# Kernel tuning notes

Measured on AMD Instinct MI355X. Metric: run time of the kernel, lower is better.

The kernel has to match this reference:

```python
import jax, jax.numpy as jnp
import numpy as np

H = 128
S = 65  # 64 board cells + 1 appended bias token


def _attn(y, wk, wq, wv):
    # y: [B, H, S]
    k = jnp.einsum('ij,bjs->bis', wk, y)
    q = jnp.einsum('ij,bjs->bis', wq, y)
    v = jnp.einsum('ij,bjs->bis', wv, y)
    kq = jnp.einsum('bis,bit->bst', k, q)          # k.T @ q -> [B, S, S]
    sm = jax.nn.softmax(kq, axis=-1)               # softmax over dim=1 of [S,S]
    return jnp.einsum('bst,bit->bsi', sm, v)       # sm @ v.T -> [B, S, H]


def setup_inputs() -> dict:
    key = jax.random.key(0)
    ks = jax.random.split(key, 17)
    B = 8192
    d = dict(
        inputs=jax.random.normal(ks[0], (1, B, 64), jnp.float32),
        embeding=jax.random.normal(ks[1], (H, S), jnp.float32),
        w_k11=jax.random.normal(ks[2], (H, H), jnp.float32),
        w_q11=jax.random.normal(ks[3], (H, H), jnp.float32),
        w_v11=jax.random.normal(ks[4], (H, H), jnp.float32),
        w_k12=jax.random.normal(ks[5], (H, H), jnp.float32),
        w_q12=jax.random.normal(ks[6], (H, H), jnp.float32),
        w_v12=jax.random.normal(ks[7], (H, H), jnp.float32),
        linear1=jax.random.normal(ks[8], (2 * H, H), jnp.float32),
        w_k21=jax.random.normal(ks[9], (H, H), jnp.float32),
        w_q21=jax.random.normal(ks[10], (H, H), jnp.float32),
        w_v21=jax.random.normal(ks[11], (H, H), jnp.float32),
        w_k22=jax.random.normal(ks[12], (H, H), jnp.float32),
        w_q22=jax.random.normal(ks[13], (H, H), jnp.float32),
        w_v22=jax.random.normal(ks[14], (H, H), jnp.float32),
        linear2=jax.random.normal(ks[15], (2 * H, H), jnp.float32),
        linear3=jax.random.normal(ks[16], (H, H // 2), jnp.float32),
        linear4=jax.random.normal(jax.random.fold_in(key, 99), (H // 2, 1), jnp.float32),
    )
    return d


def reference(inputs, embeding, w_k11, w_q11, w_v11, w_k12, w_q12, w_v12, linear1,
              w_k21, w_q21, w_v21, w_k22, w_q22, w_v22, linear2, linear3, linear4):
    xb = inputs[0]                                   # [B, 64]
    B = xb.shape[0]
    x = jnp.concatenate([xb, jnp.ones((B, 1), xb.dtype)], axis=1)  # [B, 65]
    y = embeding[None, :, :] * x[:, None, :]         # [B, H, S]

    att11 = _attn(y, w_k11, w_q11, w_v11)            # [B, S, H]
    att12 = _attn(y, w_k12, w_q12, w_v12)
    y = jnp.tanh(jnp.concatenate([att11, att12], axis=-1) @ linear1)  # [B, S, H]
    y = jnp.swapaxes(y, 1, 2)                        # [B, H, S]

    att21 = _attn(y, w_k21, w_q21, w_v21)
    att22 = _attn(y, w_k22, w_q22, w_v22)
    y = jnp.tanh(jnp.concatenate([att21, att22], axis=-1) @ linear2)  # [B, S, H]
    y = y[:, 64, :]                                  # take bias token -> [B, H]
    y = jnp.tanh(y @ linear3)                        # [B, H//2]
    score = y @ linear4                              # [B, 1]
    return score[:, 0][None, :]                      # [1, B]
```

## Files before the change

### kernel.cpp

```cpp
#include <hip/hip_runtime.h>
#include <math.h>


#define YQ(s, q) ((s) * 128 + 4 * ((q) ^ ((s) & 7)))
#define KA_STR 68
#define QA_STR 72
#define QA_BASE 4420

__global__
__attribute__((amdgpu_flat_work_group_size(512, 512)))
__attribute__((amdgpu_waves_per_eu(4, 8)))
void literal_kernel(const float* __restrict__ in0,
                    const float* __restrict__ emb,
                    const float* __restrict__ wk11, const float* __restrict__ wq11,
                    const float* __restrict__ wv11,
                    const float* __restrict__ wk12, const float* __restrict__ wq12,
                    const float* __restrict__ wv12,
                    const float* __restrict__ l1,
                    const float* __restrict__ wk21, const float* __restrict__ wq21,
                    const float* __restrict__ wv21,
                    const float* __restrict__ wk22, const float* __restrict__ wq22,
                    const float* __restrict__ wv22,
                    const float* __restrict__ l2,
                    const float* __restrict__ L3, const float* __restrict__ L4,
                    float* __restrict__ out)
{
    __shared__ __align__(16) float vsh[8320];
    __shared__ __align__(16) float R1[9028];
    __shared__ __align__(16) float k64sh[128];
    __shared__ __align__(16) float q64sh[128];
    __shared__ float kq64sh[68];
    __shared__ __align__(16) float smr[68];
    __shared__ __align__(16) float attr[128];
    __shared__ float y4sh[128];

    const int tid  = threadIdx.x;
    const int lane = tid & 63;
    const int wu   = __builtin_amdgcn_readfirstlane(tid >> 6);
    const long b   = blockIdx.x;
    const float xr = in0[b * 64 + lane];

    float* kA = R1;
    float* qA = R1 + QA_BASE;

    const int h4 = (tid & 31) * 4;
    const int sb = tid >> 5;
    float4 acc1[5];
    #pragma unroll
    for (int si = 0; si < 5; ++si) acc1[si] = make_float4(0.f, 0.f, 0.f, 0.f);

    for (int a = 0; a < 2; ++a) {
        const float* wk = a ? wk12 : wk11;
        const float* wq = a ? wq12 : wq11;
        const float* wv = a ? wv12 : wv11;

        float kqa[8];
        #pragma unroll
        for (int m = 0; m < 8; ++m) kqa[m] = 0.f;
        float kq64acc = 0.f, kqr64acc = 0.f, corner = 0.f;

        for (int p = 0; p < 2; ++p) {
            const int ip0 = p * 64 + wu * 8;
            float aK[8], aQ[8], aV[8];
            #pragma unroll
            for (int r = 0; r < 8; ++r) { aK[r] = aQ[r] = aV[r] = 0.f; }
            float acc64 = 0.f;
            {
                const int ch = lane >> 3;
                const float* Wc = (ch == 0) ? wk : ((ch == 1) ? wq : wv);
                const float* wcrow = Wc + (ip0 + (lane & 7)) * 128;
                for (int jq = 0; jq < 32; ++jq) {
                    const float* erow = emb + (jq * 4) * 65;
                    float yv[4], y64v[4];
                    #pragma unroll
                    for (int u = 0; u < 4; ++u) {
                        yv[u]   = erow[u * 65 + lane] * xr;
                        y64v[u] = erow[u * 65 + 64];
                    }
                    #pragma unroll
                    for (int r = 0; r < 8; ++r) {
                        const float* wkr = wk + (ip0 + r) * 128 + jq * 4;
                        const float* wqr = wq + (ip0 + r) * 128 + jq * 4;
                        const float* wvr = wv + (ip0 + r) * 128 + jq * 4;
                        #pragma unroll
                        for (int u = 0; u < 4; ++u) {
                            aK[r] = fmaf(wkr[u], yv[u], aK[r]);
                            aQ[r] = fmaf(wqr[u], yv[u], aQ[r]);
                            aV[r] = fmaf(wvr[u], yv[u], aV[r]);
                        }
                    }
                    if (lane < 24) {
                        float4 c0 = *(const float4*)&wcrow[jq * 4];
                        acc64 = fmaf(c0.x, y64v[0], acc64);
                        acc64 = fmaf(c0.y, y64v[1], acc64);
                        acc64 = fmaf(c0.z, y64v[2], acc64);
                        acc64 = fmaf(c0.w, y64v[3], acc64);
                    }
                }
                *(float4*)&kA[lane * KA_STR + wu * 8]     = make_float4(aK[0], aK[1], aK[2], aK[3]);
                *(float4*)&kA[lane * KA_STR + wu * 8 + 4] = make_float4(aK[4], aK[5], aK[6], aK[7]);
                *(float4*)&qA[lane * QA_STR + wu * 8]     = make_float4(aQ[0], aQ[1], aQ[2], aQ[3]);
                *(float4*)&qA[lane * QA_STR + wu * 8 + 4] = make_float4(aQ[4], aQ[5], aQ[6], aQ[7]);
                #pragma unroll
                for (int r = 0; r < 8; ++r) vsh[(ip0 + r) * 65 + lane] = aV[r];
                if (lane < 8)            k64sh[ip0 + lane] = acc64;
                else if (lane < 16)      q64sh[ip0 + (lane & 7)] = acc64;
                else if (lane < 24)      vsh[(ip0 + (lane & 7)) * 65 + 64] = acc64;
            }
            __syncthreads();

            for (int iq = 0; iq < 16; ++iq) {
                float4 qq = *(const float4*)&qA[lane * QA_STR + iq * 4];
                #pragma unroll
                for (int m = 0; m < 8; ++m) {
                    float4 kk = *(const float4*)&kA[(wu + 8 * m) * KA_STR + iq * 4];
                    kqa[m] = fmaf(kk.x, qq.x, kqa[m]);
                    kqa[m] = fmaf(kk.y, qq.y, kqa[m]);
                    kqa[m] = fmaf(kk.z, qq.z, kqa[m]);
                    kqa[m] = fmaf(kk.w, qq.w, kqa[m]);
                }
                if (wu == 0) {
                    float4 kc = *(const float4*)&k64sh[p * 64 + iq * 4];
                    float4 qc = *(const float4*)&q64sh[p * 64 + iq * 4];
                    kqr64acc = fmaf(kc.x, qq.x, kqr64acc);
                    kqr64acc = fmaf(kc.y, qq.y, kqr64acc);
                    kqr64acc = fmaf(kc.z, qq.z, kqr64acc);
                    kqr64acc = fmaf(kc.w, qq.w, kqr64acc);
                    float4 ks = *(const float4*)&kA[lane * KA_STR + iq * 4];
                    kq64acc = fmaf(ks.x, qc.x, kq64acc);
                    kq64acc = fmaf(ks.y, qc.y, kq64acc);
                    kq64acc = fmaf(ks.z, qc.z, kq64acc);
                    kq64acc = fmaf(ks.w, qc.w, kq64acc);
                    if (lane == 0) {
                        corner = fmaf(kc.x, qc.x, corner);
                        corner = fmaf(kc.y, qc.y, corner);
                        corner = fmaf(kc.z, qc.z, corner);
                        corner = fmaf(kc.w, qc.w, corner);
                    }
                }
            }
            if (p == 1 && wu == 0) {
                kq64sh[lane] = kq64acc;
                if (lane == 0) kq64sh[64] = corner;
            }
            __syncthreads();
        }

        float smv[9], sm64v[9];
        #pragma unroll
        for (int m = 0; m < 9; ++m) { smv[m] = 0.f; sm64v[m] = 0.f; }
        #pragma unroll
        for (int m = 0; m < 9; ++m) {
            if (m < 8 || wu == 0) {
                int s = (m == 8) ? 64 : (wu + 8 * m);
                float lg   = (m == 8) ? kqr64acc : kqa[m];
                float l64v = (lane == 0) ? kq64sh[s] : -3.0e38f;
                float mm = fmaxf(lg, l64v);
                #pragma unroll
                for (int off = 32; off >= 1; off >>= 1) mm = fmaxf(mm, __shfl_xor(mm, off));
                float e   = expf(lg - mm);
                float e64 = (lane == 0) ? expf(l64v - mm) : 0.f;
                float zs = e + e64;
                #pragma unroll
                for (int off = 32; off >= 1; off >>= 1) zs += __shfl_xor(zs, off);
                float inv = 1.0f / zs;
                smv[m] = e * inv;
                sm64v[m] = e64 * inv;
            }
        }
        {
            float aa0[9], aa1[9];
            #pragma unroll
            for (int m = 0; m < 9; ++m) { aa0[m] = 0.f; aa1[m] = 0.f; }
            const float* vr0 = &vsh[lane * 65];
            const float* vr1 = &vsh[(lane + 64) * 65];
            for (int t = 0; t < 64; ++t) {
                float v0 = vr0[t], v1 = vr1[t];
                #pragma unroll
                for (int m = 0; m < 9; ++m) {
                    if (m < 8 || wu == 0) {
                        float smt = __shfl(smv[m], t);
                        aa0[m] = fmaf(smt, v0, aa0[m]);
                        aa1[m] = fmaf(smt, v1, aa1[m]);
                    }
                }
            }
            float v0e = vr0[64], v1e = vr1[64];
            #pragma unroll
            for (int m = 0; m < 9; ++m) {
                if (m < 8 || wu == 0) {
                    float smt = __shfl(sm64v[m], 0);
                    aa0[m] = fmaf(smt, v0e, aa0[m]);
                    aa1[m] = fmaf(smt, v1e, aa1[m]);
                    int s = (m == 8) ? 64 : (wu + 8 * m);
                    R1[s * 128 + lane]      = aa0[m];
                    R1[s * 128 + lane + 64] = aa1[m];
                }
            }
        }
        __syncthreads();

        {
            const float* l1a = l1 + a * 16384;
            for (int i0b = 0; i0b < 128; i0b += 4) {
                float4 av0 = *(const float4*)&R1[(sb +  0) * 128 + i0b];
                float4 av1 = *(const float4*)&R1[(sb + 16) * 128 + i0b];
                float4 av2 = *(const float4*)&R1[(sb + 32) * 128 + i0b];
                float4 av3 = *(const float4*)&R1[(sb + 48) * 128 + i0b];
                float4 av4 = make_float4(0.f, 0.f, 0.f, 0.f);
                if (sb == 0) av4 = *(const float4*)&R1[64 * 128 + i0b];
                float a0[4] = { av0.x, av0.y, av0.z, av0.w };
                float a1[4] = { av1.x, av1.y, av1.z, av1.w };
                float a2[4] = { av2.x, av2.y, av2.z, av2.w };
                float a3[4] = { av3.x, av3.y, av3.z, av3.w };
                float a4[4] = { av4.x, av4.y, av4.z, av4.w };
                #pragma unroll
                for (int r = 0; r < 4; ++r) {
                    float4 lv = *(const float4*)&l1a[(i0b + r) * 128 + h4];
                    acc1[0].x = fmaf(a0[r], lv.x, acc1[0].x);
                    acc1[0].y = fmaf(a0[r], lv.y, acc1[0].y);
                    acc1[0].z = fmaf(a0[r], lv.z, acc1[0].z);
                    acc1[0].w = fmaf(a0[r], lv.w, acc1[0].w);
                    acc1[1].x = fmaf(a1[r], lv.x, acc1[1].x);
                    acc1[1].y = fmaf(a1[r], lv.y, acc1[1].y);
                    acc1[1].z = fmaf(a1[r], lv.z, acc1[1].z);
                    acc1[1].w = fmaf(a1[r], lv.w, acc1[1].w);
                    acc1[2].x = fmaf(a2[r], lv.x, acc1[2].x);
                    acc1[2].y = fmaf(a2[r], lv.y, acc1[2].y);
                    acc1[2].z = fmaf(a2[r], lv.z, acc1[2].z);
                    acc1[2].w = fmaf(a2[r], lv.w, acc1[2].w);
                    acc1[3].x = fmaf(a3[r], lv.x, acc1[3].x);
                    acc1[3].y = fmaf(a3[r], lv.y, acc1[3].y);
                    acc1[3].z = fmaf(a3[r], lv.z, acc1[3].z);
                    acc1[3].w = fmaf(a3[r], lv.w, acc1[3].w);
                    if (sb == 0) {
                        acc1[4].x = fmaf(a4[r], lv.x, acc1[4].x);
                        acc1[4].y = fmaf(a4[r], lv.y, acc1[4].y);
                        acc1[4].z = fmaf(a4[r], lv.z, acc1[4].z);
                        acc1[4].w = fmaf(a4[r], lv.w, acc1[4].w);
                    }
                }
            }
        }
        __syncthreads();
    }

    #pragma unroll
    for (int si = 0; si < 5; ++si) {
        if (si < 4 || sb == 0) {
            int s = (si == 4) ? 64 : (sb + 16 * si);
            float4 tq;
            tq.x = tanhf(acc1[si].x);
            tq.y = tanhf(acc1[si].y);
            tq.z = tanhf(acc1[si].z);
            tq.w = tanhf(acc1[si].w);
            *(float4*)&vsh[YQ(s, h4 >> 2)] = tq;
        }
    }
    __syncthreads();

    float pre2 = 0.f;
    for (int a2 = 0; a2 < 2; ++a2) {
        const float* wk2 = a2 ? wk22 : wk21;
        const float* wq2 = a2 ? wq22 : wq21;
        const float* wv2 = a2 ? wv22 : wv21;

        float v2A[8], v2B[8];
        float v2c64A = 0.f, v2c64B = 0.f;
        float kq2acc = 0.f, corner2 = 0.f;

        for (int p = 0; p < 2; ++p) {
            const int ip0 = p * 64 + wu * 8;
            float aQ[8], aV[8];
            #pragma unroll
            for (int r = 0; r < 8; ++r) { aQ[r] = aV[r] = 0.f; }
            float acc64 = 0.f;
            {
                const int ch = lane >> 3;
                const float* Wc = (ch == 0) ? wq2 : ((ch == 1) ? wv2 : wk2);
                const float* wcrow = Wc + (ip0 + (lane & 7)) * 128;
                for (int jq = 0; jq < 32; ++jq) {
                    float4 yq = *(const float4*)&vsh[YQ(lane, jq)];
                    float4 zq = *(const float4*)&vsh[YQ(64, jq)];
                    float yv[4]   = { yq.x, yq.y, yq.z, yq.w };
                    float y64v[4] = { zq.x, zq.y, zq.z, zq.w };
                    #pragma unroll
                    for (int r = 0; r < 8; ++r) {
                        const float* wqr = wq2 + (ip0 + r) * 128 + jq * 4;
                        const float* wvr = wv2 + (ip0 + r) * 128 + jq * 4;
                        #pragma unroll
                        for (int u = 0; u < 4; ++u) {
                            aQ[r] = fmaf(wqr[u], yv[u], aQ[r]);
                            aV[r] = fmaf(wvr[u], yv[u], aV[r]);
                        }
                    }
                    if (lane < 24) {
                        float4 c0 = *(const float4*)&wcrow[jq * 4];
                        acc64 = fmaf(c0.x, y64v[0], acc64);
                        acc64 = fmaf(c0.y, y64v[1], acc64);
                        acc64 = fmaf(c0.z, y64v[2], acc64);
                        acc64 = fmaf(c0.w, y64v[3], acc64);
                    }
                }
                *(float4*)&qA[lane * QA_STR + wu * 8]     = make_float4(aQ[0], aQ[1], aQ[2], aQ[3]);
                *(float4*)&qA[lane * QA_STR + wu * 8 + 4] = make_float4(aQ[4], aQ[5], aQ[6], aQ[7]);
                if (lane < 8)            q64sh[ip0 + lane] = acc64;
                else if (lane < 16)      { if (p == 0) v2c64A = acc64; else v2c64B = acc64; }
                else if (lane < 24)      k64sh[ip0 + (lane & 7)] = acc64;
                #pragma unroll
                for (int r = 0; r < 8; ++r) {
                    if (p == 0) v2A[r] = aV[r]; else v2B[r] = aV[r];
                }
            }
            __syncthreads();

            if (wu == 0) {
                for (int iq = 0; iq < 16; ++iq) {
                    float4 qq = *(const float4*)&qA[lane * QA_STR + iq * 4];
                    float4 kk = *(const float4*)&k64sh[p * 64 + iq * 4];
                    kq2acc = fmaf(kk.x, qq.x, kq2acc);
                    kq2acc = fmaf(kk.y, qq.y, kq2acc);
                    kq2acc = fmaf(kk.z, qq.z, kq2acc);
                    kq2acc = fmaf(kk.w, qq.w, kq2acc);
                    if (lane == 0) {
                        float4 qz = *(const float4*)&q64sh[p * 64 + iq * 4];
                        corner2 = fmaf(kk.x, qz.x, corner2);
                        corner2 = fmaf(kk.y, qz.y, corner2);
                        corner2 = fmaf(kk.z, qz.z, corner2);
                        corner2 = fmaf(kk.w, qz.w, corner2);
                    }
                }
            }
            __syncthreads();
        }

        if (wu == 0) {
            float lg   = kq2acc;
            float l64v = (lane == 0) ? corner2 : -3.0e38f;
            float mm = fmaxf(lg, l64v);
            #pragma unroll
            for (int off = 32; off >= 1; off >>= 1) mm = fmaxf(mm, __shfl_xor(mm, off));
            float e   = expf(lg - mm);
            float e64 = (lane == 0) ? expf(l64v - mm) : 0.f;
            float zs = e + e64;
            #pragma unroll
            for (int off = 32; off >= 1; off >>= 1) zs += __shfl_xor(zs, off);
            float inv = 1.0f / zs;
            smr[lane] = e * inv;
            if (lane == 0) smr[64] = e64 * inv;
        }
        __syncthreads();

        {
            float sv = smr[lane];
            float part[16];
            #pragma unroll
            for (int r = 0; r < 8; ++r) { part[r] = sv * v2A[r]; part[8 + r] = sv * v2B[r]; }
            #pragma unroll
            for (int off = 32; off >= 1; off >>= 1) {
                #pragma unroll
                for (int r = 0; r < 16; ++r) part[r] += __shfl_xor(part[r], off);
            }
            float sm64 = smr[64];
            int rr = lane & 15;
            float c64A = __shfl(v2c64A, 8 + (lane & 7));
            float c64B = __shfl(v2c64B, 8 + (lane & 7));
            float myval = 0.f;
            #pragma unroll
            for (int r = 0; r < 16; ++r) myval = (rr == r) ? part[r] : myval;
            if (lane < 16) {
                int irow = (rr < 8) ? (wu * 8 + rr) : (64 + wu * 8 + (rr - 8));
                float c64 = (rr < 8) ? c64A : c64B;
                attr[irow] = myval + sm64 * c64;
            }
        }
        __syncthreads();

        {
            const int hh = tid & 127, cc = tid >> 7;
            const float* l2a = l2 + a2 * 16384;
            float pp = 0.f;
            #pragma unroll
            for (int g = 0; g < 8; ++g) {
                int i = cc * 32 + 4 * g;
                float4 av = *(const float4*)&attr[i];
                pp = fmaf(av.x, l2a[(i + 0) * 128 + hh], pp);
                pp = fmaf(av.y, l2a[(i + 1) * 128 + hh], pp);
                pp = fmaf(av.z, l2a[(i + 2) * 128 + hh], pp);
                pp = fmaf(av.w, l2a[(i + 3) * 128 + hh], pp);
            }
            R1[cc * 128 + hh] = pp;
        }
        __syncthreads();
        if (tid < 128) {
            float red = R1[tid];
            #pragma unroll
            for (int c = 1; c < 4; ++c) red += R1[c * 128 + tid];
            pre2 += red;
        }
        __syncthreads();
    }

    if (tid < 128) y4sh[tid] = tanhf(pre2);
    __syncthreads();

    {
        const int oo = tid & 63, cc = tid >> 6;
        float pp = 0.f;
        #pragma unroll
        for (int u = 0; u < 16; ++u) {
            int h = cc * 16 + u;
            pp = fmaf(y4sh[h], L3[h * 64 + oo], pp);
        }
        R1[cc * 64 + oo] = pp;
    }
    __syncthreads();
    if (tid < 64) {
        float t3 = R1[tid];
        #pragma unroll
        for (int c = 1; c < 8; ++c) t3 += R1[c * 64 + tid];
        float y5 = tanhf(t3);
        float sc = y5 * L4[tid];
        #pragma unroll
        for (int off = 32; off >= 1; off >>= 1) sc += __shfl_xor(sc, off);
        if (tid == 0) out[b] = sc;
    }
}

extern "C" void kernel_launch(void* const* d_in, const int* in_sizes, int n_in,
                              void* d_out, int out_size, void* d_ws, size_t ws_size,
                              hipStream_t stream) {
    const float* in0  = (const float*)d_in[0];
    const float* emb  = (const float*)d_in[1];
    const float* wk11 = (const float*)d_in[2];
    const float* wq11 = (const float*)d_in[3];
    const float* wv11 = (const float*)d_in[4];
    const float* wk12 = (const float*)d_in[5];
    const float* wq12 = (const float*)d_in[6];
    const float* wv12 = (const float*)d_in[7];
    const float* l1   = (const float*)d_in[8];
    const float* wk21 = (const float*)d_in[9];
    const float* wq21 = (const float*)d_in[10];
    const float* wv21 = (const float*)d_in[11];
    const float* wk22 = (const float*)d_in[12];
    const float* wq22 = (const float*)d_in[13];
    const float* wv22 = (const float*)d_in[14];
    const float* l2   = (const float*)d_in[15];
    const float* l3   = (const float*)d_in[16];
    const float* l4   = (const float*)d_in[17];
    float* out = (float*)d_out;

    int B = in_sizes[0] / 64;

    literal_kernel<<<B, 512, 0, stream>>>(in0, emb,
                                          wk11, wq11, wv11, wk12, wq12, wv12, l1,
                                          wk21, wq21, wv21, wk22, wq22, wv22, l2,
                                          l3, l4, out);
}
```

Baseline: 5.880 ms.

## Split projection, softmax and reduction loops into smaller chunks to cut register pressure

Splits the per-warp K/Q/V projection accumulators into two halves of four rows, computes the softmax-times-V product in three chunks of three rows, and splits the final 16-way shuffle reduction into two 8-way passes. Each change lowers how many live VGPRs the kernel needs. The waves-per-EU hint is pinned to 4 so the compiler can spend the freed registers without aiming for higher occupancy. The cost is that embedding and y loads are read twice, once per half, and there are more loop passes.

```diff
diff --git a/kernel.cpp b/kernel.cpp
--- a/kernel.cpp
+++ b/kernel.cpp
@@ -9,7 +9,7 @@
 
 __global__
 __attribute__((amdgpu_flat_work_group_size(512, 512)))
-__attribute__((amdgpu_waves_per_eu(4, 8)))
+__attribute__((amdgpu_waves_per_eu(4, 4)))
 void literal_kernel(const float* __restrict__ in0,
                     const float* __restrict__ emb,
                     const float* __restrict__ wk11, const float* __restrict__ wq11,
@@ -61,27 +61,28 @@
 
         for (int p = 0; p < 2; ++p) {
             const int ip0 = p * 64 + wu * 8;
-            float aK[8], aQ[8], aV[8];
-            #pragma unroll
-            for (int r = 0; r < 8; ++r) { aK[r] = aQ[r] = aV[r] = 0.f; }
-            float acc64 = 0.f;
-            {
+
+            #pragma unroll
+            for (int half = 0; half < 2; ++half) {
+                const int rb = ip0 + half * 4;
+                float aK[4] = {0.f,0.f,0.f,0.f};
+                float aQ[4] = {0.f,0.f,0.f,0.f};
+                float aV[4] = {0.f,0.f,0.f,0.f};
+                float acc64 = 0.f;
                 const int ch = lane >> 3;
                 const float* Wc = (ch == 0) ? wk : ((ch == 1) ? wq : wv);
                 const float* wcrow = Wc + (ip0 + (lane & 7)) * 128;
+
                 for (int jq = 0; jq < 32; ++jq) {
                     const float* erow = emb + (jq * 4) * 65;
-                    float yv[4], y64v[4];
-                    #pragma unroll
-                    for (int u = 0; u < 4; ++u) {
-                        yv[u]   = erow[u * 65 + lane] * xr;
-                        y64v[u] = erow[u * 65 + 64];
-                    }
-                    #pragma unroll
-                    for (int r = 0; r < 8; ++r) {
-                        const float* wkr = wk + (ip0 + r) * 128 + jq * 4;
-                        const float* wqr = wq + (ip0 + r) * 128 + jq * 4;
-                        const float* wvr = wv + (ip0 + r) * 128 + jq * 4;
+                    float yv[4];
+                    #pragma unroll
+                    for (int u = 0; u < 4; ++u) yv[u] = erow[u * 65 + lane] * xr;
+                    #pragma unroll
+                    for (int r = 0; r < 4; ++r) {
+                        const float* wkr = wk + (rb + r) * 128 + jq * 4;
+                        const float* wqr = wq + (rb + r) * 128 + jq * 4;
+                        const float* wvr = wv + (rb + r) * 128 + jq * 4;
                         #pragma unroll
                         for (int u = 0; u < 4; ++u) {
                             aK[r] = fmaf(wkr[u], yv[u], aK[r]);
@@ -89,23 +90,23 @@
                             aV[r] = fmaf(wvr[u], yv[u], aV[r]);
                         }
                     }
-                    if (lane < 24) {
+                    if (half == 0 && lane < 24) {
                         float4 c0 = *(const float4*)&wcrow[jq * 4];
-                        acc64 = fmaf(c0.x, y64v[0], acc64);
-                        acc64 = fmaf(c0.y, y64v[1], acc64);
-                        acc64 = fmaf(c0.z, y64v[2], acc64);
-                        acc64 = fmaf(c0.w, y64v[3], acc64);
-                    }
-                }
-                *(float4*)&kA[lane * KA_STR + wu * 8]     = make_float4(aK[0], aK[1], aK[2], aK[3]);
-                *(float4*)&kA[lane * KA_STR + wu * 8 + 4] = make_float4(aK[4], aK[5], aK[6], aK[7]);
-                *(float4*)&qA[lane * QA_STR + wu * 8]     = make_float4(aQ[0], aQ[1], aQ[2], aQ[3]);
-                *(float4*)&qA[lane * QA_STR + wu * 8 + 4] = make_float4(aQ[4], aQ[5], aQ[6], aQ[7]);
-                #pragma unroll
-                for (int r = 0; r < 8; ++r) vsh[(ip0 + r) * 65 + lane] = aV[r];
-                if (lane < 8)            k64sh[ip0 + lane] = acc64;
-                else if (lane < 16)      q64sh[ip0 + (lane & 7)] = acc64;
-                else if (lane < 24)      vsh[(ip0 + (lane & 7)) * 65 + 64] = acc64;
+                        acc64 = fmaf(c0.x, erow[0 * 65 + 64], acc64);
+                        acc64 = fmaf(c0.y, erow[1 * 65 + 64], acc64);
+                        acc64 = fmaf(c0.z, erow[2 * 65 + 64], acc64);
+                        acc64 = fmaf(c0.w, erow[3 * 65 + 64], acc64);
+                    }
+                }
+                *(float4*)&kA[lane * KA_STR + wu * 8 + half * 4] = make_float4(aK[0], aK[1], aK[2], aK[3]);
+                *(float4*)&qA[lane * QA_STR + wu * 8 + half * 4] = make_float4(aQ[0], aQ[1], aQ[2], aQ[3]);
+                #pragma unroll
+                for (int r = 0; r < 4; ++r) vsh[(rb + r) * 65 + lane] = aV[r];
+                if (half == 0) {
+                    if (lane < 8)            k64sh[ip0 + lane] = acc64;
+                    else if (lane < 16)      q64sh[ip0 + (lane & 7)] = acc64;
+                    else if (lane < 24)      vsh[(ip0 + (lane & 7)) * 65 + 64] = acc64;
+                }
             }
             __syncthreads();
 
@@ -119,13 +120,16 @@
                     kqa[m] = fmaf(kk.z, qq.z, kqa[m]);
                     kqa[m] = fmaf(kk.w, qq.w, kqa[m]);
                 }
-                if (wu == 0) {
+            }
+            if (wu == 0) {
+                for (int iq = 0; iq < 16; ++iq) {
+                    float4 qq = *(const float4*)&qA[lane * QA_STR + iq * 4];
                     float4 kc = *(const float4*)&k64sh[p * 64 + iq * 4];
-                    float4 qc = *(const float4*)&q64sh[p * 64 + iq * 4];
                     kqr64acc = fmaf(kc.x, qq.x, kqr64acc);
                     kqr64acc = fmaf(kc.y, qq.y, kqr64acc);
                     kqr64acc = fmaf(kc.z, qq.z, kqr64acc);
                     kqr64acc = fmaf(kc.w, qq.w, kqr64acc);
+                    float4 qc = *(const float4*)&q64sh[p * 64 + iq * 4];
                     float4 ks = *(const float4*)&kA[lane * KA_STR + iq * 4];
                     kq64acc = fmaf(ks.x, qc.x, kq64acc);
                     kq64acc = fmaf(ks.y, qc.y, kq64acc);
@@ -138,63 +142,65 @@
                         corner = fmaf(kc.w, qc.w, corner);
                     }
                 }
-            }
-            if (p == 1 && wu == 0) {
-                kq64sh[lane] = kq64acc;
-                if (lane == 0) kq64sh[64] = corner;
+                if (p == 1) {
+                    kq64sh[lane] = kq64acc;
+                    if (lane == 0) kq64sh[64] = corner;
+                }
             }
             __syncthreads();
         }
 
-        float smv[9], sm64v[9];
-        #pragma unroll
-        for (int m = 0; m < 9; ++m) { smv[m] = 0.f; sm64v[m] = 0.f; }
-        #pragma unroll
-        for (int m = 0; m < 9; ++m) {
-            if (m < 8 || wu == 0) {
-                int s = (m == 8) ? 64 : (wu + 8 * m);
-                float lg   = (m == 8) ? kqr64acc : kqa[m];
-                float l64v = (lane == 0) ? kq64sh[s] : -3.0e38f;
-                float mm = fmaxf(lg, l64v);
-                #pragma unroll
-                for (int off = 32; off >= 1; off >>= 1) mm = fmaxf(mm, __shfl_xor(mm, off));
-                float e   = expf(lg - mm);
-                float e64 = (lane == 0) ? expf(l64v - mm) : 0.f;
-                float zs = e + e64;
-                #pragma unroll
-                for (int off = 32; off >= 1; off >>= 1) zs += __shfl_xor(zs, off);
-                float inv = 1.0f / zs;
-                smv[m] = e * inv;
-                sm64v[m] = e64 * inv;
-            }
-        }
         {
-            float aa0[9], aa1[9];
-            #pragma unroll
-            for (int m = 0; m < 9; ++m) { aa0[m] = 0.f; aa1[m] = 0.f; }
             const float* vr0 = &vsh[lane * 65];
             const float* vr1 = &vsh[(lane + 64) * 65];
-            for (int t = 0; t < 64; ++t) {
-                float v0 = vr0[t], v1 = vr1[t];
-                #pragma unroll
-                for (int m = 0; m < 9; ++m) {
+            #pragma unroll
+            for (int mc = 0; mc < 3; ++mc) {
+                float smv[3] = {0.f, 0.f, 0.f}, sm64v[3] = {0.f, 0.f, 0.f};
+                #pragma unroll
+                for (int mm = 0; mm < 3; ++mm) {
+                    const int m = mc * 3 + mm;
                     if (m < 8 || wu == 0) {
-                        float smt = __shfl(smv[m], t);
-                        aa0[m] = fmaf(smt, v0, aa0[m]);
-                        aa1[m] = fmaf(smt, v1, aa1[m]);
-                    }
-                }
-            }
-            float v0e = vr0[64], v1e = vr1[64];
-            #pragma unroll
-            for (int m = 0; m < 9; ++m) {
-                if (m < 8 || wu == 0) {
-                    float smt = __shfl(sm64v[m], 0);
-                    aa0[m] = fmaf(smt, v0e, aa0[m]);
-                    aa1[m] = fmaf(smt, v1e, aa1[m]);
-                    int s = (m == 8) ? 64 : (wu + 8 * m);
-                    R1[s * 128 + lane]      = aa0[m];
-                    R1[s * 128 + lane + 64] = aa1[m];
+                        int s = (m == 8) ? 64 : (wu + 8 * m);
+                        float lg   = (m == 8) ? kqr64acc : kqa[m];
+                        float l64v = (lane == 0) ? kq64sh[s] : -3.0e38f;
+                        float mmx = fmaxf(lg, l64v);
+                        #pragma unroll
+                        for (int off = 32; off >= 1; off >>= 1) mmx = fmaxf(mmx, __shfl_xor(mmx, off));
+                        float e   = expf(lg - mmx);
+                        float e64 = (lane == 0) ? expf(l64v - mmx) : 0.f;
+                        float zs = e + e64;
+                        #pragma unroll
+                        for (int off = 32; off >= 1; off >>= 1) zs += __shfl_xor(zs, off);
+                        float inv = 1.0f / zs;
+                        smv[mm] = e * inv;
+                        sm64v[mm] = e64 * inv;
+                    }
+                }
+                float aa0[3] = {0.f, 0.f, 0.f}, aa1[3] = {0.f, 0.f, 0.f};
+                for (int t = 0; t < 64; ++t) {
+                    float v0 = vr0[t], v1 = vr1[t];
+                    #pragma unroll
+                    for (int mm = 0; mm < 3; ++mm) {
+                        const int m = mc * 3 + mm;
+                        if (m < 8 || wu == 0) {
+                            float smt = __shfl(smv[mm], t);
+                            aa0[mm] = fmaf(smt, v0, aa0[mm]);
+                            aa1[mm] = fmaf(smt, v1, aa1[mm]);
+                        }
+                    }
+                }
+                float v0e = vr0[64], v1e = vr1[64];
+                #pragma unroll
+                for (int mm = 0; mm < 3; ++mm) {
+                    const int m = mc * 3 + mm;
+                    if (m < 8 || wu == 0) {
+                        float smt = __shfl(sm64v[mm], 0);
+                        aa0[mm] = fmaf(smt, v0e, aa0[mm]);
+                        aa1[mm] = fmaf(smt, v1e, aa1[mm]);
+                        int s = (m == 8) ? 64 : (wu + 8 * m);
+                        R1[s * 128 + lane]      = aa0[mm];
+                        R1[s * 128 + lane + 64] = aa1[mm];
+                    }
                 }
             }
         }
@@ -271,45 +277,48 @@
 
         for (int p = 0; p < 2; ++p) {
             const int ip0 = p * 64 + wu * 8;
-            float aQ[8], aV[8];
-            #pragma unroll
-            for (int r = 0; r < 8; ++r) { aQ[r] = aV[r] = 0.f; }
-            float acc64 = 0.f;
-            {
+            #pragma unroll
+            for (int half = 0; half < 2; ++half) {
+                const int rb = ip0 + half * 4;
+                float aQ[4] = {0.f,0.f,0.f,0.f};
+                float aV[4] = {0.f,0.f,0.f,0.f};
+                float acc64 = 0.f;
                 const int ch = lane >> 3;
                 const float* Wc = (ch == 0) ? wq2 : ((ch == 1) ? wv2 : wk2);
                 const float* wcrow = Wc + (ip0 + (lane & 7)) * 128;
+
                 for (int jq = 0; jq < 32; ++jq) {
                     float4 yq = *(const float4*)&vsh[YQ(lane, jq)];
-                    float4 zq = *(const float4*)&vsh[YQ(64, jq)];
-                    float yv[4]   = { yq.x, yq.y, yq.z, yq.w };
-                    float y64v[4] = { zq.x, zq.y, zq.z, zq.w };
-                    #pragma unroll
-                    for (int r = 0; r < 8; ++r) {
-                        const float* wqr = wq2 + (ip0 + r) * 128 + jq * 4;
-                        const float* wvr = wv2 + (ip0 + r) * 128 + jq * 4;
+                    float yv[4] = { yq.x, yq.y, yq.z, yq.w };
+                    #pragma unroll
+                    for (int r = 0; r < 4; ++r) {
+                        const float* wqr = wq2 + (rb + r) * 128 + jq * 4;
+                        const float* wvr = wv2 + (rb + r) * 128 + jq * 4;
                         #pragma unroll
                         for (int u = 0; u < 4; ++u) {
                             aQ[r] = fmaf(wqr[u], yv[u], aQ[r]);
                             aV[r] = fmaf(wvr[u], yv[u], aV[r]);
                         }
                     }
-                    if (lane < 24) {
+                    if (half == 0 && lane < 24) {
+                        float4 zq = *(const float4*)&vsh[YQ(64, jq)];
                         float4 c0 = *(const float4*)&wcrow[jq * 4];
-                        acc64 = fmaf(c0.x, y64v[0], acc64);
-                        acc64 = fmaf(c0.y, y64v[1], acc64);
-                        acc64 = fmaf(c0.z, y64v[2], acc64);
-                        acc64 = fmaf(c0.w, y64v[3], acc64);
-                    }
-                }
-                *(float4*)&qA[lane * QA_STR + wu * 8]     = make_float4(aQ[0], aQ[1], aQ[2], aQ[3]);
-                *(float4*)&qA[lane * QA_STR + wu * 8 + 4] = make_float4(aQ[4], aQ[5], aQ[6], aQ[7]);
-                if (lane < 8)            q64sh[ip0 + lane] = acc64;
-                else if (lane < 16)      { if (p == 0) v2c64A = acc64; else v2c64B = acc64; }
-                else if (lane < 24)      k64sh[ip0 + (lane & 7)] = acc64;
-                #pragma unroll
-                for (int r = 0; r < 8; ++r) {
-                    if (p == 0) v2A[r] = aV[r]; else v2B[r] = aV[r];
+                        acc64 = fmaf(c0.x, zq.x, acc64);
+                        acc64 = fmaf(c0.y, zq.y, acc64);
+                        acc64 = fmaf(c0.z, zq.z, acc64);
+                        acc64 = fmaf(c0.w, zq.w, acc64);
+                    }
+                }
+                *(float4*)&qA[lane * QA_STR + wu * 8 + half * 4] = make_float4(aQ[0], aQ[1], aQ[2], aQ[3]);
+                #pragma unroll
+                for (int r = 0; r < 4; ++r) {
+                    if (p == 0) v2A[half * 4 + r] = aV[r];
+                    else        v2B[half * 4 + r] = aV[r];
+                }
+                if (half == 0) {
+                    if (lane < 8)            q64sh[ip0 + lane] = acc64;
+                    else if (lane < 16)      { if (p == 0) v2c64A = acc64; else v2c64B = acc64; }
+                    else if (lane < 24)      k64sh[ip0 + (lane & 7)] = acc64;
                 }
             }
             __syncthreads();
@@ -353,25 +362,36 @@
 
         {
             float sv = smr[lane];
-            float part[16];
-            #pragma unroll
-            for (int r = 0; r < 8; ++r) { part[r] = sv * v2A[r]; part[8 + r] = sv * v2B[r]; }
-            #pragma unroll
-            for (int off = 32; off >= 1; off >>= 1) {
-                #pragma unroll
-                for (int r = 0; r < 16; ++r) part[r] += __shfl_xor(part[r], off);
-            }
             float sm64 = smr[64];
-            int rr = lane & 15;
-            float c64A = __shfl(v2c64A, 8 + (lane & 7));
-            float c64B = __shfl(v2c64B, 8 + (lane & 7));
-            float myval = 0.f;
-            #pragma unroll
-            for (int r = 0; r < 16; ++r) myval = (rr == r) ? part[r] : myval;
-            if (lane < 16) {
-                int irow = (rr < 8) ? (wu * 8 + rr) : (64 + wu * 8 + (rr - 8));
-                float c64 = (rr < 8) ? c64A : c64B;
-                attr[irow] = myval + sm64 * c64;
+            {
+                float part[8];
+                #pragma unroll
+                for (int r = 0; r < 8; ++r) part[r] = sv * v2A[r];
+                #pragma unroll
+                for (int off = 32; off >= 1; off >>= 1) {
+                    #pragma unroll
+                    for (int r = 0; r < 8; ++r) part[r] += __shfl_xor(part[r], off);
+                }
+                float c64 = __shfl(v2c64A, 8 + (lane & 7));
+                float myval = part[0];
+                #pragma unroll
+                for (int r = 1; r < 8; ++r) myval = ((lane & 7) == r) ? part[r] : myval;
+                if (lane < 8) attr[wu * 8 + lane] = myval + sm64 * c64;
+            }
+            {
+                float part[8];
+                #pragma unroll
+                for (int r = 0; r < 8; ++r) part[r] = sv * v2B[r];
+                #pragma unroll
+                for (int off = 32; off >= 1; off >>= 1) {
+                    #pragma unroll
+                    for (int r = 0; r < 8; ++r) part[r] += __shfl_xor(part[r], off);
+                }
+                float c64 = __shfl(v2c64B, 8 + (lane & 7));
+                float myval = part[0];
+                #pragma unroll
+                for (int r = 1; r < 8; ++r) myval = ((lane & 7) == r) ? part[r] : myval;
+                if (lane < 8) attr[64 + wu * 8 + lane] = myval + sm64 * c64;
             }
         }
         __syncthreads();
```

New measurement: 6.364 ms. 8.2% more time.

## Reassociate second-layer V projection and move bias-token linear1 row to separate pass

Applied to the files above, without the earlier changes.

In the second attention stage only the bias-token row is needed, so the full V projection is no longer computed. The kernel first reduces softmax weights against y (u = y·sm), then applies Wv once as a 128x128 matvec, and drops the per-lane aV accumulators and shuffle reductions. The bias-token row of the first linear1 product is also pulled out of the main tiled loop into a dedicated 128-thread matvec, which removes the divergent sb==0 branch and one accumulator set. The cost is extra serial loops on only 128 threads plus additional barriers.

```diff
diff --git a/kernel.cpp b/kernel.cpp
--- a/kernel.cpp
+++ b/kernel.cpp
@@ -45,9 +45,9 @@
 
     const int h4 = (tid & 31) * 4;
     const int sb = tid >> 5;
-    float4 acc1[5];
+    float4 acc1[4];
     #pragma unroll
-    for (int si = 0; si < 5; ++si) acc1[si] = make_float4(0.f, 0.f, 0.f, 0.f);
+    for (int si = 0; si < 4; ++si) acc1[si] = make_float4(0.f, 0.f, 0.f, 0.f);
 
     for (int a = 0; a < 2; ++a) {
         const float* wk = a ? wk12 : wk11;
@@ -71,12 +71,9 @@
                 const float* wcrow = Wc + (ip0 + (lane & 7)) * 128;
                 for (int jq = 0; jq < 32; ++jq) {
                     const float* erow = emb + (jq * 4) * 65;
-                    float yv[4], y64v[4];
+                    float yv[4];
                     #pragma unroll
-                    for (int u = 0; u < 4; ++u) {
-                        yv[u]   = erow[u * 65 + lane] * xr;
-                        y64v[u] = erow[u * 65 + 64];
-                    }
+                    for (int u = 0; u < 4; ++u) yv[u] = erow[u * 65 + lane] * xr;
                     #pragma unroll
                     for (int r = 0; r < 8; ++r) {
                         const float* wkr = wk + (ip0 + r) * 128 + jq * 4;
@@ -91,10 +88,10 @@
                     }
                     if (lane < 24) {
                         float4 c0 = *(const float4*)&wcrow[jq * 4];
-                        acc64 = fmaf(c0.x, y64v[0], acc64);
-                        acc64 = fmaf(c0.y, y64v[1], acc64);
-                        acc64 = fmaf(c0.z, y64v[2], acc64);
-                        acc64 = fmaf(c0.w, y64v[3], acc64);
+                        acc64 = fmaf(c0.x, erow[0 * 65 + 64], acc64);
+                        acc64 = fmaf(c0.y, erow[1 * 65 + 64], acc64);
+                        acc64 = fmaf(c0.z, erow[2 * 65 + 64], acc64);
+                        acc64 = fmaf(c0.w, erow[3 * 65 + 64], acc64);
                     }
                 }
                 *(float4*)&kA[lane * KA_STR + wu * 8]     = make_float4(aK[0], aK[1], aK[2], aK[3]);
@@ -200,6 +197,8 @@
         }
         __syncthreads();
 
+        if (a == 0 && tid < 128) attr[tid] = R1[64 * 128 + tid];
+
         {
             const float* l1a = l1 + a * 16384;
             for (int i0b = 0; i0b < 128; i0b += 4) {
@@ -207,13 +206,10 @@
                 float4 av1 = *(const float4*)&R1[(sb + 16) * 128 + i0b];
                 float4 av2 = *(const float4*)&R1[(sb + 32) * 128 + i0b];
                 float4 av3 = *(const float4*)&R1[(sb + 48) * 128 + i0b];
-                float4 av4 = make_float4(0.f, 0.f, 0.f, 0.f);
-                if (sb == 0) av4 = *(const float4*)&R1[64 * 128 + i0b];
                 float a0[4] = { av0.x, av0.y, av0.z, av0.w };
                 float a1[4] = { av1.x, av1.y, av1.z, av1.w };
                 float a2[4] = { av2.x, av2.y, av2.z, av2.w };
                 float a3[4] = { av3.x, av3.y, av3.z, av3.w };
-                float a4[4] = { av4.x, av4.y, av4.z, av4.w };
                 #pragma unroll
                 for (int r = 0; r < 4; ++r) {
                     float4 lv = *(const float4*)&l1a[(i0b + r) * 128 + h4];
@@ -233,29 +229,29 @@
                     acc1[3].y = fmaf(a3[r], lv.y, acc1[3].y);
                     acc1[3].z = fmaf(a3[r], lv.z, acc1[3].z);
                     acc1[3].w = fmaf(a3[r], lv.w, acc1[3].w);
-                    if (sb == 0) {
-                        acc1[4].x = fmaf(a4[r], lv.x, acc1[4].x);
-                        acc1[4].y = fmaf(a4[r], lv.y, acc1[4].y);
-                        acc1[4].z = fmaf(a4[r], lv.z, acc1[4].z);
-                        acc1[4].w = fmaf(a4[r], lv.w, acc1[4].w);
-                    }
-                }
-            }
-        }
-        __syncthreads();
-    }
-
+                }
+            }
+        }
+        __syncthreads();
+    }
+
+    if (tid < 128) {
+        const float* l1a0 = l1;
+        const float* l1a1 = l1 + 16384;
+        float acc = 0.f;
+        for (int i = 0; i < 128; ++i) acc = fmaf(attr[i],        l1a0[i * 128 + tid], acc);
+        for (int i = 0; i < 128; ++i) acc = fmaf(R1[64*128 + i], l1a1[i * 128 + tid], acc);
+        vsh[YQ(64, tid >> 2) + (tid & 3)] = tanhf(acc);
+    }
     #pragma unroll
-    for (int si = 0; si < 5; ++si) {
-        if (si < 4 || sb == 0) {
-            int s = (si == 4) ? 64 : (sb + 16 * si);
-            float4 tq;
-            tq.x = tanhf(acc1[si].x);
-            tq.y = tanhf(acc1[si].y);
-            tq.z = tanhf(acc1[si].z);
-            tq.w = tanhf(acc1[si].w);
-            *(float4*)&vsh[YQ(s, h4 >> 2)] = tq;
-        }
+    for (int si = 0; si < 4; ++si) {
+        int s = sb + 16 * si;
+        float4 tq;
+        tq.x = tanhf(acc1[si].x);
+        tq.y = tanhf(acc1[si].y);
+        tq.z = tanhf(acc1[si].z);
+        tq.w = tanhf(acc1[si].w);
+        *(float4*)&vsh[YQ(s, h4 >> 2)] = tq;
     }
     __syncthreads();
 
@@ -265,52 +261,41 @@
         const float* wq2 = a2 ? wq22 : wq21;
         const float* wv2 = a2 ? wv22 : wv21;
 
-        float v2A[8], v2B[8];
-        float v2c64A = 0.f, v2c64B = 0.f;
         float kq2acc = 0.f, corner2 = 0.f;
 
         for (int p = 0; p < 2; ++p) {
             const int ip0 = p * 64 + wu * 8;
-            float aQ[8], aV[8];
-            #pragma unroll
-            for (int r = 0; r < 8; ++r) { aQ[r] = aV[r] = 0.f; }
+            float aQ[8];
+            #pragma unroll
+            for (int r = 0; r < 8; ++r) aQ[r] = 0.f;
             float acc64 = 0.f;
             {
                 const int ch = lane >> 3;
-                const float* Wc = (ch == 0) ? wq2 : ((ch == 1) ? wv2 : wk2);
+                const float* Wc = (ch == 0) ? wq2 : wk2;
                 const float* wcrow = Wc + (ip0 + (lane & 7)) * 128;
                 for (int jq = 0; jq < 32; ++jq) {
                     float4 yq = *(const float4*)&vsh[YQ(lane, jq)];
-                    float4 zq = *(const float4*)&vsh[YQ(64, jq)];
-                    float yv[4]   = { yq.x, yq.y, yq.z, yq.w };
-                    float y64v[4] = { zq.x, zq.y, zq.z, zq.w };
+                    float yv[4] = { yq.x, yq.y, yq.z, yq.w };
                     #pragma unroll
                     for (int r = 0; r < 8; ++r) {
                         const float* wqr = wq2 + (ip0 + r) * 128 + jq * 4;
-                        const float* wvr = wv2 + (ip0 + r) * 128 + jq * 4;
                         #pragma unroll
-                        for (int u = 0; u < 4; ++u) {
+                        for (int u = 0; u < 4; ++u)
                             aQ[r] = fmaf(wqr[u], yv[u], aQ[r]);
-                            aV[r] = fmaf(wvr[u], yv[u], aV[r]);
-                        }
-                    }
-                    if (lane < 24) {
+                    }
+                    if (lane < 16) {
+                        float4 zq = *(const float4*)&vsh[YQ(64, jq)];
                         float4 c0 = *(const float4*)&wcrow[jq * 4];
-                        acc64 = fmaf(c0.x, y64v[0], acc64);
-                        acc64 = fmaf(c0.y, y64v[1], acc64);
-                        acc64 = fmaf(c0.z, y64v[2], acc64);
-                        acc64 = fmaf(c0.w, y64v[3], acc64);
+                        acc64 = fmaf(c0.x, zq.x, acc64);
+                        acc64 = fmaf(c0.y, zq.y, acc64);
+                        acc64 = fmaf(c0.z, zq.z, acc64);
+                        acc64 = fmaf(c0.w, zq.w, acc64);
                     }
                 }
                 *(float4*)&qA[lane * QA_STR + wu * 8]     = make_float4(aQ[0], aQ[1], aQ[2], aQ[3]);
                 *(float4*)&qA[lane * QA_STR + wu * 8 + 4] = make_float4(aQ[4], aQ[5], aQ[6], aQ[7]);
                 if (lane < 8)            q64sh[ip0 + lane] = acc64;
-                else if (lane < 16)      { if (p == 0) v2c64A = acc64; else v2c64B = acc64; }
-                else if (lane < 24)      k64sh[ip0 + (lane & 7)] = acc64;
-                #pragma unroll
-                for (int r = 0; r < 8; ++r) {
-                    if (p == 0) v2A[r] = aV[r]; else v2B[r] = aV[r];
-                }
+                else if (lane < 16)      k64sh[ip0 + (lane & 7)] = acc64;
             }
             __syncthreads();
 
@@ -351,28 +336,25 @@
         }
         __syncthreads();
 
-        {
-            float sv = smr[lane];
-            float part[16];
-            #pragma unroll
-            for (int r = 0; r < 8; ++r) { part[r] = sv * v2A[r]; part[8 + r] = sv * v2B[r]; }
-            #pragma unroll
-            for (int off = 32; off >= 1; off >>= 1) {
-                #pragma unroll
-                for (int r = 0; r < 16; ++r) part[r] += __shfl_xor(part[r], off);
-            }
-            float sm64 = smr[64];
-            int rr = lane & 15;
-            float c64A = __shfl(v2c64A, 8 + (lane & 7));
-            float c64B = __shfl(v2c64B, 8 + (lane & 7));
-            float myval = 0.f;
-            #pragma unroll
-            for (int r = 0; r < 16; ++r) myval = (rr == r) ? part[r] : myval;
-            if (lane < 16) {
-                int irow = (rr < 8) ? (wu * 8 + rr) : (64 + wu * 8 + (rr - 8));
-                float c64 = (rr < 8) ? c64A : c64B;
-                attr[irow] = myval + sm64 * c64;
-            }
+        if (tid < 128) {
+            float uacc = 0.f;
+            for (int t = 0; t <= 64; ++t)
+                uacc = fmaf(smr[t], vsh[YQ(t, tid >> 2) + (tid & 3)], uacc);
+            k64sh[tid] = uacc;
+        }
+        __syncthreads();
+
+        if (tid < 128) {
+            const float* wvrow = wv2 + tid * 128;
+            float acc = 0.f;
+            for (int h0 = 0; h0 < 128; h0 += 4) {
+                float4 wq4 = *(const float4*)&wvrow[h0];
+                acc = fmaf(wq4.x, k64sh[h0 + 0], acc);
+                acc = fmaf(wq4.y, k64sh[h0 + 1], acc);
+                acc = fmaf(wq4.z, k64sh[h0 + 2], acc);
+                acc = fmaf(wq4.w, k64sh[h0 + 3], acc);
+            }
+            attr[tid] = acc;
         }
         __syncthreads();
 
```

Measured after the change: 5.402 ms. -8.1%, faster.
